# Optimization experiments

Hardware: AMD Instinct MI355X
Metric: run time of the kernel (lower is better)

## Reference

```python
import jax, jax.numpy as jnp
import numpy as np

G = 8          # deformable groups
K = 9          # 3x3 kernel points
MAXR = 10.0    # max_residue_magnitude


def conv2d(x, w, b):
    # x: [B,Cin,H,W], w: [Cout,Cin,3,3], SAME padding, stride 1
    y = jax.lax.conv_general_dilated(x, w, (1, 1), ((1, 1), (1, 1)),
                                     dimension_numbers=('NCHW', 'OIHW', 'NCHW'))
    return y + b[None, :, None, None]


def lrelu(x):
    return jnp.where(x >= 0, x, 0.1 * x)


def offset_branch(x, ws, bs):
    for w, b in zip(ws[:-1], bs[:-1]):
        x = lrelu(conv2d(x, w, b))
    return conv2d(x, ws[-1], bs[-1])


def mdcn(x, offset, mask, w, b):
    # Modulated deformable conv, 3x3, stride 1, pad 1, dilation 1, groups=1.
    # offset: [B, G*K*2, H, W] ordered (g, k, (y,x)); mask: [B, G*K, H, W]
    B, C, H, W = x.shape
    Cg = C // G
    off = offset.reshape(B, G, K, 2, H, W)
    m = mask.reshape(B, G, K, H, W)
    ky = (jnp.arange(K) // 3 - 1).astype(x.dtype)   # kernel dy, pad=1
    kx = (jnp.arange(K) % 3 - 1).astype(x.dtype)    # kernel dx
    hy = jnp.arange(H, dtype=x.dtype)
    wx = jnp.arange(W, dtype=x.dtype)
    py = hy[None, None, None, :, None] + ky[None, None, :, None, None] + off[:, :, :, 0]  # [B,G,K,H,W]
    px = wx[None, None, None, None, :] + kx[None, None, :, None, None] + off[:, :, :, 1]
    y0f = jnp.floor(py); x0f = jnp.floor(px)
    ly = py - y0f; lx = px - x0f
    y0 = y0f.astype(jnp.int32); x0 = x0f.astype(jnp.int32)
    xf = x.reshape(B, G, Cg, H * W)

    def gather(yi, xi):
        valid = ((yi >= 0) & (yi < H) & (xi >= 0) & (xi < W)).astype(x.dtype)
        yc = jnp.clip(yi, 0, H - 1)
        xc = jnp.clip(xi, 0, W - 1)
        idx = (yc * W + xc).reshape(B, G, 1, K * H * W)
        v = jnp.take_along_axis(xf, idx, axis=3).reshape(B, G, Cg, K, H, W)
        return v * valid.reshape(B, G, 1, K, H, W)

    ly_ = ly[:, :, None]; lx_ = lx[:, :, None]  # [B,G,1,K,H,W]
    samp = (gather(y0, x0) * (1 - ly_) * (1 - lx_)
            + gather(y0, x0 + 1) * (1 - ly_) * lx_
            + gather(y0 + 1, x0) * ly_ * (1 - lx_)
            + gather(y0 + 1, x0 + 1) * ly_ * lx_)
    samp = samp * m[:, :, None]                 # modulation
    wr = w.reshape(w.shape[0], G, Cg, K)        # [Cout,G,Cg,K]
    return jnp.einsum('ogck,bgckhw->bohw', wr, samp) + b[None, :, None, None]


def setup_inputs():
    key = jax.random.key(0)
    ks = jax.random.split(key, 40)
    B, C, H, W = 1, 64, 256, 256
    s = 0.05
    inp = {
        'feat_prev': jax.random.normal(ks[0], (B, C, H, W), jnp.float32),
        'feat_next': jax.random.normal(ks[1], (B, C, H, W), jnp.float32),
        'extra_feat_prev': jax.random.normal(ks[2], (B, 2 * C, H, W), jnp.float32),
        'extra_feat_next': jax.random.normal(ks[3], (B, 2 * C, H, W), jnp.float32),
        'flow_prev': jax.random.normal(ks[4], (B, 2, H, W), jnp.float32),
        'flow_next': jax.random.normal(ks[5], (B, 2, H, W), jnp.float32),
    }
    shapes = [(C, 2 * C, 3, 3), (C, C, 3, 3), (C, C, 3, 3), (27 * G, C, 3, 3)]
    i = 6
    for pre in ('off1', 'off2'):
        for j, sh in enumerate(shapes):
            inp[f'{pre}_w{j}'] = jax.random.normal(ks[i], sh, jnp.float32) * s; i += 1
            inp[f'{pre}_b{j}'] = jax.random.normal(ks[i], (sh[0],), jnp.float32) * s; i += 1
    inp['dcn1_w'] = jax.random.normal(ks[i], (C, C, 3, 3), jnp.float32) * s; i += 1
    inp['dcn1_b'] = jax.random.normal(ks[i], (C,), jnp.float32) * s; i += 1
    inp['dcn2_w'] = jax.random.normal(ks[i], (C, C, 3, 3), jnp.float32) * s; i += 1
    inp['dcn2_b'] = jax.random.normal(ks[i], (C,), jnp.float32) * s; i += 1
    inp['fus_w'] = jax.random.normal(ks[i], (C, 2 * C, 3, 3), jnp.float32) * s; i += 1
    inp['fus_b'] = jax.random.normal(ks[i], (C,), jnp.float32) * s
    return inp


def reference(feat_prev, feat_next, extra_feat_prev, extra_feat_next, flow_prev, flow_next,
              off1_w0, off1_b0, off1_w1, off1_b1, off1_w2, off1_b2, off1_w3, off1_b3,
              off2_w0, off2_b0, off2_w1, off2_b1, off2_w2, off2_b2, off2_w3, off2_b3,
              dcn1_w, dcn1_b, dcn2_w, dcn2_b, fus_w, fus_b):
    def branch(feat, extra, flow, ws, bs, dw, db):
        out = offset_branch(extra, ws, bs)
        o1, o2, msk = jnp.split(out, 3, axis=1)
        off = MAXR * jnp.tanh(jnp.concatenate([o1, o2], axis=1))
        off = off + jnp.tile(flow[:, ::-1], (1, off.shape[1] // 2, 1, 1))  # flip(1).repeat
        msk = jax.nn.sigmoid(msk)
        return mdcn(feat, off, msk, dw, db)

    fp = branch(feat_prev, extra_feat_prev, flow_prev,
                [off1_w0, off1_w1, off1_w2, off1_w3], [off1_b0, off1_b1, off1_b2, off1_b3],
                dcn1_w, dcn1_b)
    fn = branch(feat_next, extra_feat_next, flow_next,
                [off2_w0, off2_w1, off2_w2, off2_w3], [off2_b0, off2_b1, off2_b2, off2_b3],
                dcn2_w, dcn2_b)
    return conv2d(jnp.concatenate([fp, fn], axis=1), fus_w, fus_b)
```

## Files before the change

### kernel.cpp

```cpp
#include <hip/hip_runtime.h>
#include <cstddef>
#include <cstdint>

constexpr int IMG = 256;
constexpr int NPIX = 65536;
constexpr int PW = 258;
constexpr size_t PREC = (size_t)PW * PW;

typedef _Float16 h8 __attribute__((ext_vector_type(8)));
typedef float f32x4 __attribute__((ext_vector_type(4)));

template<int CIN>
__device__ __forceinline__ void zero_pad_rec(int i, _Float16* buf)
{
  constexpr int Q = CIN / 8;
  if (i >= 1028 * Q) return;
  int pr = i / Q, qi = i - pr * Q;
  int rec;
  if (pr < 258) rec = pr;
  else if (pr < 516) rec = 257 * 258 + (pr - 258);
  else { int j = pr - 516; rec = (1 + (j >> 1)) * 258 + ((j & 1) ? 257 : 0); }
  *reinterpret_cast<uint4*>(&buf[(size_t)rec * CIN + qi * 8]) = uint4{0, 0, 0, 0};
}

template<int CIN>
__global__ __launch_bounds__(256) void zeropad_k(_Float16* __restrict__ buf)
{
  zero_pad_rec<CIN>(blockIdx.x * 256 + threadIdx.x, buf);
}

template<int CIN>
__global__ __launch_bounds__(256) void prep_hwc_k(
    const float* __restrict__ in0, const float* __restrict__ in1,
    _Float16* __restrict__ out0, _Float16* __restrict__ out1)
{
  const int z = blockIdx.z;
  const float* in = z ? in1 : in0;
  _Float16* out = z ? out1 : out0;
  int b = blockIdx.x;
  if (b >= 256) { zero_pad_rec<CIN>((b - 256) * 256 + threadIdx.x, out); return; }
  int pix = b * 256 + threadIdx.x;
  int py = pix >> 8, px = pix & 255;
  size_t rec = ((size_t)(py + 1) * PW + px + 1) * CIN;
#pragma unroll
  for (int c0 = 0; c0 < CIN; c0 += 8) {
    _Float16 t[8];
#pragma unroll
    for (int j = 0; j < 8; ++j)
      t[j] = (_Float16)in[(size_t)(c0 + j) * NPIX + pix];
    *reinterpret_cast<uint4*>(&out[rec + c0]) = *reinterpret_cast<uint4*>(t);
  }
}

__device__ __forceinline__ void wfrag(
    const float* __restrict__ w, int cin_tot, int cin_off, int KC, int NBF,
    int nvalid, int idx, _Float16* __restrict__ oHi, _Float16* __restrict__ oLo)
{
  int l = idx & 63;
  int r = idx >> 6;
  int fg = r % NBF; r /= NBF;
  int c = r % KC;
  int t = r / KC;
  int n = fg * 16 + (l & 15);
  int cinb = c * 32 + (l >> 4) * 8;
  _Float16 vh[8], vl[8];
#pragma unroll
  for (int j = 0; j < 8; ++j) {
    float x = 0.f;
    if (n < nvalid) x = w[((size_t)n * cin_tot + cin_off + cinb + j) * 9 + t];
    vh[j] = (_Float16)x;
    vl[j] = (_Float16)(x - (float)vh[j]);
  }
  *reinterpret_cast<uint4*>(oHi + (size_t)idx * 8) = *reinterpret_cast<uint4*>(vh);
  if (oLo)
    *reinterpret_cast<uint4*>(oLo + (size_t)idx * 8) = *reinterpret_cast<uint4*>(vl);
}

__global__ __launch_bounds__(256) void wprep_all_k(
    const float* __restrict__ w0, const float* __restrict__ w1,
    const float* __restrict__ w2, const float* __restrict__ w3,
    const float* __restrict__ wf, const float* __restrict__ dw,
    _Float16* b0h, _Float16* b0l, _Float16* b1h, _Float16* b1l,
    _Float16* b2h, _Float16* b2l, _Float16* b3h, _Float16* b3l,
    _Float16* bfh, _Float16* __restrict__ wB)
{
  int idx = blockIdx.x * 256 + threadIdx.x;
  if (idx < 9216)       wfrag(w0, 128, 0, 4, 4, 64, idx, b0h, b0l);
  else if (idx < 13824) wfrag(w1, 64, 0, 2, 4, 64, idx - 9216, b1h, b1l);
  else if (idx < 18432) wfrag(w2, 64, 0, 2, 4, 64, idx - 13824, b2h, b2l);
  else if (idx < 36864) wfrag(w3, 64, 0, 2, 16, 216, idx - 18432, b3h, b3l);
  else if (idx < 41472) {
    int i = idx - 36864;
    int l = i & 63;
    int r = i >> 6;
    int f = r & 3;
    int p = r >> 2;
    int t = p * 4 + (l >> 4);
    int g = (t * 57) >> 9;
    int k = t - 9 * g;
    int n = f * 16 + (l & 15);
    _Float16 v[8];
#pragma unroll
    for (int j = 0; j < 8; ++j)
      v[j] = (_Float16)dw[(size_t)n * 576 + g * 72 + j * 9 + k];
    *reinterpret_cast<uint4*>(wB + (size_t)i * 8) = *reinterpret_cast<uint4*>(v);
  }
  else if (wf && idx < 50688)
    wfrag(wf, 128, 0, 4, 4, 64, idx - 41472, bfh, nullptr);
}

template<int CIN, int EPI, bool DBL, typename OT>
__global__ __launch_bounds__(256) void conv_mfma_k(
    const _Float16* __restrict__ act0, const _Float16* __restrict__ act1,
    const _Float16* __restrict__ wHi0, const _Float16* __restrict__ wHi1,
    const _Float16* __restrict__ wLo0, const _Float16* __restrict__ wLo1,
    const float* __restrict__ bias0, const float* __restrict__ bias1,
    OT* __restrict__ out0, OT* __restrict__ out1, int ncout, int NBF)
{
  constexpr int Q = CIN / 8;
  constexpr int KC = CIN / 32;
  constexpr int NT = DBL ? 2 : 1;
  constexpr int NREC = 198;
  __shared__ __align__(16) _Float16 sA[NREC * CIN];

  const int z = blockIdx.z;
  const _Float16* __restrict__ act = z ? act1 : act0;
  const _Float16* __restrict__ wHi = z ? wHi1 : wHi0;
  const _Float16* __restrict__ wLo = z ? wLo1 : wLo0;
  const float* __restrict__ bias = z ? bias1 : bias0;
  OT* __restrict__ out = z ? out1 : out0;

  const int tid = threadIdx.x;
  const int lane = tid & 63;
  const int wv = tid >> 6;
  const int b = blockIdx.x;
  const int inner = b >> 3;
  const int y = (b & 7) * 32 + (inner & 31);
  const int x0 = (inner >> 5) << 6;
  const int n0 = blockIdx.y << 6;

  for (int i = tid; i < NREC * Q; i += 256) {
    int rec = i / Q, q = i - rec * Q;
    int seg = rec / 66, xr = rec - seg * 66;
    size_t g = ((size_t)(y + seg) * PW + x0 + xr) * CIN + q * 8;
    int slot = (q + rec) & (Q - 1);
    *reinterpret_cast<uint4*>(&sA[rec * CIN + slot * 8]) =
        *reinterpret_cast<const uint4*>(&act[g]);
  }

  const int fgb = (n0 >> 4) + wv;
  auto bload = [&](int t, int c, const _Float16* src) {
    return *reinterpret_cast<const h8*>(
        &src[((((size_t)t * KC + c) * NBF + fgb) * 64 + lane) * 8]);
  };
  h8 Bn[KC][NT];
#pragma unroll
  for (int c = 0; c < KC; ++c) {
    Bn[c][0] = bload(0, c, wHi);
    if (DBL) Bn[c][1] = bload(0, c, wLo);
  }

  f32x4 acc[4];
#pragma unroll
  for (int a = 0; a < 4; ++a) acc[a] = f32x4{0.f, 0.f, 0.f, 0.f};
  __syncthreads();

  const int m = lane & 15, kq = lane >> 4;
#pragma unroll 1
  for (int t = 0; t < 9; ++t) {
    h8 Bc[KC][NT];
#pragma unroll
    for (int c = 0; c < KC; ++c) {
      Bc[c][0] = Bn[c][0];
      if (DBL) Bc[c][1] = Bn[c][1];
    }
    if (t < 8) {
#pragma unroll
      for (int c = 0; c < KC; ++c) {
        Bn[c][0] = bload(t + 1, c, wHi);
        if (DBL) Bn[c][1] = bload(t + 1, c, wLo);
      }
    }
    const int lrb = (t / 3) * 66 + (t % 3) + m;
#pragma unroll
    for (int c = 0; c < KC; ++c) {
      const int q = c * 4 + kq;
#pragma unroll
      for (int mf = 0; mf < 4; ++mf) {
        int lr = lrb + mf * 16;
        int slot = (q + lr) & (Q - 1);
        h8 ah = *reinterpret_cast<const h8*>(&sA[lr * CIN + slot * 8]);
        acc[mf] = __builtin_amdgcn_mfma_f32_16x16x32_f16(
            ah, Bc[c][0], acc[mf], 0, 0, 0);
        if (DBL)
          acc[mf] = __builtin_amdgcn_mfma_f32_16x16x32_f16(
              ah, Bc[c][1], acc[mf], 0, 0, 0);
      }
    }
  }

  if (EPI == 0) {
    const int ch = wv * 16 + m;
    const float bv = bias[ch];
#pragma unroll
    for (int mf = 0; mf < 4; ++mf)
#pragma unroll
      for (int r = 0; r < 4; ++r) {
        int p = mf * 16 + kq * 4 + r;
        float v = acc[mf][r] + bv;
        v = (v >= 0.f) ? v : 0.1f * v;
        reinterpret_cast<_Float16*>(out)[((size_t)(y + 1) * PW + x0 + p + 1) * 64 + ch] =
            (_Float16)v;
      }
  } else {
    __syncthreads();
    float* sF = reinterpret_cast<float*>(sA);
    const int nl = wv * 16 + m;
#pragma unroll
    for (int mf = 0; mf < 4; ++mf) {
      int ml = mf * 16 + kq * 4;
      f32x4 v = acc[mf];
      float bv = (n0 + nl < ncout) ? bias[n0 + nl] : 0.f;
      v[0] += bv; v[1] += bv; v[2] += bv; v[3] += bv;
      *reinterpret_cast<f32x4*>(&sF[nl * 68 + ml]) = v;
    }
    __syncthreads();
    for (int i = tid; i < 1024; i += 256) {
      int row = i >> 4, cx = (i & 15) * 4;
      int gc = n0 + row;
      if (gc < ncout) {
        f32x4 v = *reinterpret_cast<f32x4*>(&sF[row * 68 + cx]);
        size_t ob = (size_t)gc * NPIX + (size_t)y * IMG + x0 + cx;
        if (sizeof(OT) == 2) {
          _Float16 t4[4] = {(_Float16)v[0], (_Float16)v[1],
                            (_Float16)v[2], (_Float16)v[3]};
          *reinterpret_cast<uint2*>(reinterpret_cast<_Float16*>(out) + ob) =
              *reinterpret_cast<uint2*>(t4);
        } else {
          *reinterpret_cast<f32x4*>(reinterpret_cast<float*>(out) + ob) = v;
        }
      }
    }
  }
}

__global__ __launch_bounds__(256) void featg_k(
    const float* __restrict__ in0, const float* __restrict__ in1,
    _Float16* __restrict__ out0, _Float16* __restrict__ out1)
{
  const int z = blockIdx.z;
  const float* in = z ? in1 : in0;
  _Float16* out = z ? out1 : out0;
  int pix = blockIdx.x * 256 + threadIdx.x;
#pragma unroll
  for (int g = 0; g < 8; ++g) {
    _Float16 t[8];
#pragma unroll
    for (int c = 0; c < 8; ++c)
      t[c] = (_Float16)in[(size_t)(g * 8 + c) * NPIX + pix];
    *reinterpret_cast<uint4*>(&out[((size_t)g * NPIX + pix) * 8]) =
        *reinterpret_cast<uint4*>(t);
  }
}

struct GS {
  h8 a, b, c, d;
  _Float16 w00, w01, w10, w11;
  float r0, r1, r2;
  h8 bf0, bf1, bf2, bf3;
};

__global__ __launch_bounds__(256, 8) void mdcn_mfma_k(
    const _Float16* __restrict__ featG0, const _Float16* __restrict__ featG1,
    const _Float16* __restrict__ o2160, const _Float16* __restrict__ o2161,
    const float* __restrict__ flow0, const float* __restrict__ flow1,
    const _Float16* __restrict__ wB0, const _Float16* __restrict__ wB1,
    const float* __restrict__ bias0, const float* __restrict__ bias1,
    _Float16* __restrict__ actF)
{
  const int z = blockIdx.z;
  const char* __restrict__ featGc =
      reinterpret_cast<const char*>(z ? featG1 : featG0);
  const char* __restrict__ o216c =
      reinterpret_cast<const char*>(z ? o2161 : o2160);
  const float* __restrict__ flow = z ? flow1 : flow0;
  const char* __restrict__ wBc = reinterpret_cast<const char*>(z ? wB1 : wB0);
  const float* __restrict__ bias = z ? bias1 : bias0;
  const int zoff = z << 6;

  const int tid = threadIdx.x;
  const int lane = tid & 63;
  const int wv = tid >> 6;
  const int b = blockIdx.x;
  const int inner = b >> 3;
  const int row = (b & 7) * 32 + (inner & 31);
  const int xseg = inner >> 5;
  const int m = lane & 15;
  const int tq = lane >> 4;
  const int xw = xseg * 64 + wv * 16;
  const int x = xw + m;
  const int pix = row * 256 + x;

  const float fy = flow[NPIX + pix];
  const float fx = flow[pix];
  const float rowf = (float)row, xf = (float)x;

  f32x4 acc[4];
#pragma unroll
  for (int f = 0; f < 4; ++f) acc[f] = f32x4{0.f, 0.f, 0.f, 0.f};

  uint32_t ro0 = ((uint32_t)(2 * tq) * NPIX + (uint32_t)pix) * 2;
  uint32_t ro2 = ((uint32_t)(144 + tq) * NPIX + (uint32_t)pix) * 2;
  auto rawloadv = [&](float& a0, float& a1, float& a2) {
    a0 = (float)*reinterpret_cast<const _Float16*>(o216c + ro0);
    a1 = (float)*reinterpret_cast<const _Float16*>(o216c + ro0 + NPIX * 2);
    a2 = (float)*reinterpret_cast<const _Float16*>(o216c + ro2);
    ro0 += 8u * NPIX * 2;
    ro2 += 4u * NPIX * 2;
  };

  auto setup = [&](int p, float s0, float s1, float s2, GS& o) {
    const int t = p * 4 + tq;
    const int g = (t * 57) >> 9;
    const int k = t - 9 * g;
    const int kd = (k * 11) >> 5;
    const int km = k - 3 * kd;
    const float mm = __builtin_amdgcn_rcpf(1.f + __expf(-s2));
    const float e0 = __expf(2.f * s0);
    const float e1 = __expf(2.f * s1);
    const float th0 = 1.f - 2.f * __builtin_amdgcn_rcpf(e0 + 1.f);
    const float th1 = 1.f - 2.f * __builtin_amdgcn_rcpf(e1 + 1.f);
    const float pyf = rowf + (float)(kd - 1) + 10.f * th0 + fy;
    const float pxf = xf + (float)(km - 1) + 10.f * th1 + fx;
    const float y0f = floorf(pyf), x0f = floorf(pxf);
    const float ly = pyf - y0f, lx = pxf - x0f;
    const int y0 = (int)y0f, x0i = (int)x0f;
    const int y1 = y0 + 1, x1 = x0i + 1;
    const bool vy0 = (unsigned)y0 < (unsigned)IMG, vy1 = (unsigned)y1 < (unsigned)IMG;
    const bool vx0 = (unsigned)x0i < (unsigned)IMG, vx1 = (unsigned)x1 < (unsigned)IMG;
    const int y0c = min(max(y0, 0), IMG - 1), y1c = min(max(y1, 0), IMG - 1);
    const int x0c = min(max(x0i, 0), IMG - 1), x1c = min(max(x1, 0), IMG - 1);
    const float oy = 1.f - ly, ox = 1.f - lx;
    const float py0 = oy * mm, py1 = ly * mm;
    const float w00 = (vy0 && vx0) ? py0 * ox : 0.f;
    const float w01 = (vy0 && vx1) ? py0 * lx : 0.f;
    const float w10 = (vy1 && vx0) ? py1 * ox : 0.f;
    const float w11 = (vy1 && vx1) ? py1 * lx : 0.f;
    o.w00 = (_Float16)w00; o.w01 = (_Float16)w01;
    o.w10 = (_Float16)w10; o.w11 = (_Float16)w11;
    const uint32_t gb = ((uint32_t)g << 16);
    const uint32_t ry0 = gb + ((uint32_t)y0c << 8);
    const uint32_t ry1 = gb + ((uint32_t)y1c << 8);
    o.a = *reinterpret_cast<const h8*>(featGc + ((ry0 + x0c) << 4));
    o.b = *reinterpret_cast<const h8*>(featGc + ((ry0 + x1c) << 4));
    o.c = *reinterpret_cast<const h8*>(featGc + ((ry1 + x0c) << 4));
    o.d = *reinterpret_cast<const h8*>(featGc + ((ry1 + x1c) << 4));
  };

  const uint32_t lane16 = (uint32_t)lane * 16;
  auto bfload = [&](int p, GS& o) {
    const uint32_t w = (uint32_t)p * 4096 + lane16;
    o.bf0 = *reinterpret_cast<const h8*>(wBc + w);
    o.bf1 = *reinterpret_cast<const h8*>(wBc + w + 1024);
    o.bf2 = *reinterpret_cast<const h8*>(wBc + w + 2048);
    o.bf3 = *reinterpret_cast<const h8*>(wBc + w + 3072);
  };

  auto consume = [&](GS& cur) {
    h8 af = cur.a * cur.w00 + cur.b * cur.w01 +
            cur.c * cur.w10 + cur.d * cur.w11;
    acc[0] = __builtin_amdgcn_mfma_f32_16x16x32_f16(af, cur.bf0, acc[0], 0, 0, 0);
    acc[1] = __builtin_amdgcn_mfma_f32_16x16x32_f16(af, cur.bf1, acc[1], 0, 0, 0);
    acc[2] = __builtin_amdgcn_mfma_f32_16x16x32_f16(af, cur.bf2, acc[2], 0, 0, 0);
    acc[3] = __builtin_amdgcn_mfma_f32_16x16x32_f16(af, cur.bf3, acc[3], 0, 0, 0);
  };

  auto body = [&](int p, GS& cur, GS& nxt) {
    setup(p + 1, nxt.r0, nxt.r1, nxt.r2, nxt);
    rawloadv(cur.r0, cur.r1, cur.r2);
    bfload(p + 1, nxt);
    consume(cur);
  };

  GS A, B;
  {
    float t0, t1, t2;
    rawloadv(t0, t1, t2);
    rawloadv(B.r0, B.r1, B.r2);
    bfload(0, A);
    setup(0, t0, t1, t2, A);
  }

#pragma unroll 1
  for (int it = 0; it < 8; ++it) {
    body(2 * it, A, B);
    body(2 * it + 1, B, A);
  }
  setup(17, B.r0, B.r1, B.r2, B);
  bfload(17, B);
  consume(A);
  consume(B);

  const size_t rb = ((size_t)(row + 1) * PW + xw + 1) * 128 + zoff;
#pragma unroll
  for (int f = 0; f < 4; ++f) {
    const int ch = f * 16 + m;
    const float bv = bias[ch];
#pragma unroll
    for (int r = 0; r < 4; ++r)
      actF[rb + (size_t)(tq * 4 + r) * 128 + ch] = (_Float16)(acc[f][r] + bv);
  }
}

extern "C" void kernel_launch(void* const* d_in, const int* in_sizes, int n_in,
                              void* d_out, int out_size, void* d_ws, size_t ws_size,
                              hipStream_t stream)
{
  const float* feat[2]  = {(const float*)d_in[0], (const float*)d_in[1]};
  const float* extra[2] = {(const float*)d_in[2], (const float*)d_in[3]};
  const float* flow[2]  = {(const float*)d_in[4], (const float*)d_in[5]};
  const float* ow[2][4];
  const float* ob[2][4];
  for (int br = 0; br < 2; ++br)
    for (int j = 0; j < 4; ++j) {
      ow[br][j] = (const float*)d_in[6 + br * 8 + j * 2];
      ob[br][j] = (const float*)d_in[6 + br * 8 + j * 2 + 1];
    }
  const float* dcnw[2] = {(const float*)d_in[22], (const float*)d_in[24]};
  const float* dcnb[2] = {(const float*)d_in[23], (const float*)d_in[25]};
  const float* fusw = (const float*)d_in[26];
  const float* fusb = (const float*)d_in[27];

  char* wsb = (char*)d_ws;
  size_t off = 0;
  auto alloc = [&](size_t bytes) {
    void* p = wsb + off;
    off += (bytes + 255) & ~(size_t)255;
    return p;
  };
  _Float16* R1 = (_Float16*)alloc(PREC * 128 * 2 * 2);
  _Float16* actI0 = R1;
  _Float16* actI1 = R1 + PREC * 128;
  _Float16* actB0 = R1;
  _Float16* actB1 = R1 + PREC * 64;
  _Float16* actF  = R1;
  _Float16* R2 = (_Float16*)alloc(PREC * 64 * 2 * 2);
  _Float16* actA0 = R2;
  _Float16* actA1 = R2 + PREC * 64;
  _Float16* featG0 = R2;
  _Float16* featG1 = R2 + PREC * 64;
  _Float16* o2160 = (_Float16*)alloc((size_t)216 * NPIX * 2 * 2);
  _Float16* o2161 = o2160 + (size_t)216 * NPIX;
  _Float16* wB0 = (_Float16*)alloc(73728 * 2);
  _Float16* wB1 = wB0 + 36864;
  _Float16* wb0h[2] = {(_Float16*)alloc(147456), (_Float16*)alloc(147456)};
  _Float16* wb0l[2] = {(_Float16*)alloc(147456), (_Float16*)alloc(147456)};
  _Float16* wb1h[2] = {(_Float16*)alloc(73728), (_Float16*)alloc(73728)};
  _Float16* wb1l[2] = {(_Float16*)alloc(73728), (_Float16*)alloc(73728)};
  _Float16* wb2h[2] = {(_Float16*)alloc(73728), (_Float16*)alloc(73728)};
  _Float16* wb2l[2] = {(_Float16*)alloc(73728), (_Float16*)alloc(73728)};
  _Float16* wb3h[2] = {(_Float16*)alloc(294912), (_Float16*)alloc(294912)};
  _Float16* wb3l[2] = {(_Float16*)alloc(294912), (_Float16*)alloc(294912)};
  _Float16* wbFh = (_Float16*)alloc(147456);
  float* outp = (float*)d_out;

  dim3 blk256(256);
  zeropad_k<64><<<dim3(33), blk256, 0, stream>>>(actA0);
  zeropad_k<64><<<dim3(33), blk256, 0, stream>>>(actA1);

  wprep_all_k<<<dim3(198), blk256, 0, stream>>>(
      ow[0][0], ow[0][1], ow[0][2], ow[0][3], fusw, dcnw[0],
      wb0h[0], wb0l[0], wb1h[0], wb1l[0], wb2h[0], wb2l[0],
      wb3h[0], wb3l[0], wbFh, wB0);
  wprep_all_k<<<dim3(162), blk256, 0, stream>>>(
      ow[1][0], ow[1][1], ow[1][2], ow[1][3], nullptr, dcnw[1],
      wb0h[1], wb0l[1], wb1h[1], wb1l[1], wb2h[1], wb2l[1],
      wb3h[1], wb3l[1], nullptr, wB1);

  prep_hwc_k<128><<<dim3(321, 1, 2), blk256, 0, stream>>>(
      extra[0], extra[1], actI0, actI1);

  conv_mfma_k<128, 0, true, _Float16><<<dim3(1024, 1, 2), blk256, 0, stream>>>(
      actI0, actI1, wb0h[0], wb0h[1], wb0l[0], wb0l[1],
      ob[0][0], ob[1][0], actA0, actA1, 64, 4);
  zeropad_k<64><<<dim3(33), blk256, 0, stream>>>(actB0);
  zeropad_k<64><<<dim3(33), blk256, 0, stream>>>(actB1);
  conv_mfma_k<64, 0, true, _Float16><<<dim3(1024, 1, 2), blk256, 0, stream>>>(
      actA0, actA1, wb1h[0], wb1h[1], wb1l[0], wb1l[1],
      ob[0][1], ob[1][1], actB0, actB1, 64, 4);
  conv_mfma_k<64, 0, true, _Float16><<<dim3(1024, 1, 2), blk256, 0, stream>>>(
      actB0, actB1, wb2h[0], wb2h[1], wb2l[0], wb2l[1],
      ob[0][2], ob[1][2], actA0, actA1, 64, 4);
  zeropad_k<128><<<dim3(65), blk256, 0, stream>>>(actF);
  conv_mfma_k<64, 1, true, _Float16><<<dim3(1024, 4, 2), blk256, 0, stream>>>(
      actA0, actA1, wb3h[0], wb3h[1], wb3l[0], wb3l[1],
      ob[0][3], ob[1][3], o2160, o2161, 216, 16);

  featg_k<<<dim3(256, 1, 2), blk256, 0, stream>>>(
      feat[0], feat[1], featG0, featG1);
  mdcn_mfma_k<<<dim3(1024, 1, 2), blk256, 0, stream>>>(
      featG0, featG1, o2160, o2161, flow[0], flow[1],
      wB0, wB1, dcnb[0], dcnb[1], actF);

  conv_mfma_k<128, 1, false, float><<<dim3(1024, 1, 1), blk256, 0, stream>>>(
      actF, actF, wbFh, wbFh, nullptr, nullptr,
      fusb, fusb, outp, outp, 64, 4);
}
```

Baseline: 531.0 us.

## Stage MDCN weight fragments through triple-buffered LDS shared across waves

Each wave used to load the full 4 KB weight B-fragment for every kernel step from global memory into registers. Now the four waves each load a quarter of it, store it into a three-slot shared-memory ring, and every wave reads the whole fragment back from LDS before its MFMAs. This removes the redundant per-wave global weight traffic and the register copies of the fragments held in the pipelined state struct. In exchange it adds a block-wide barrier at every step, which can stall waves that would otherwise overlap their gather latency. The launch-bounds occupancy hint is also lowered from 8 to 4.

```diff
diff --git a/kernel.cpp b/kernel.cpp
--- a/kernel.cpp
+++ b/kernel.cpp
@@ -267,10 +267,9 @@
   h8 a, b, c, d;
   _Float16 w00, w01, w10, w11;
   float r0, r1, r2;
-  h8 bf0, bf1, bf2, bf3;
 };
 
-__global__ __launch_bounds__(256, 8) void mdcn_mfma_k(
+__global__ __launch_bounds__(256, 4) void mdcn_mfma_k(
     const _Float16* __restrict__ featG0, const _Float16* __restrict__ featG1,
     const _Float16* __restrict__ o2160, const _Float16* __restrict__ o2161,
     const float* __restrict__ flow0, const float* __restrict__ flow1,
@@ -278,6 +277,8 @@
     const float* __restrict__ bias0, const float* __restrict__ bias1,
     _Float16* __restrict__ actF)
 {
+  __shared__ __align__(16) _Float16 sWB[3 * 2048];
+
   const int z = blockIdx.z;
   const char* __restrict__ featGc =
       reinterpret_cast<const char*>(z ? featG1 : featG0);
@@ -304,6 +305,9 @@
   const float fy = flow[NPIX + pix];
   const float fx = flow[pix];
   const float rowf = (float)row, xf = (float)x;
+  const uint32_t wvb = (uint32_t)wv << 10;
+  const uint32_t lane16 = (uint32_t)lane * 16;
+  const int wvh = wv << 9;
 
   f32x4 acc[4];
 #pragma unroll
@@ -357,49 +361,58 @@
     o.d = *reinterpret_cast<const h8*>(featGc + ((ry1 + x1c) << 4));
   };
 
-  const uint32_t lane16 = (uint32_t)lane * 16;
-  auto bfload = [&](int p, GS& o) {
-    const uint32_t w = (uint32_t)p * 4096 + lane16;
-    o.bf0 = *reinterpret_cast<const h8*>(wBc + w);
-    o.bf1 = *reinterpret_cast<const h8*>(wBc + w + 1024);
-    o.bf2 = *reinterpret_cast<const h8*>(wBc + w + 2048);
-    o.bf3 = *reinterpret_cast<const h8*>(wBc + w + 3072);
-  };
-
-  auto consume = [&](GS& cur) {
+  auto consume = [&](GS& cur, int bufi) {
+    const _Float16* wp = &sWB[bufi * 2048 + lane * 8];
+    h8 bf0 = *reinterpret_cast<const h8*>(wp);
+    h8 bf1 = *reinterpret_cast<const h8*>(wp + 512);
+    h8 bf2 = *reinterpret_cast<const h8*>(wp + 1024);
+    h8 bf3 = *reinterpret_cast<const h8*>(wp + 1536);
     h8 af = cur.a * cur.w00 + cur.b * cur.w01 +
             cur.c * cur.w10 + cur.d * cur.w11;
-    acc[0] = __builtin_amdgcn_mfma_f32_16x16x32_f16(af, cur.bf0, acc[0], 0, 0, 0);
-    acc[1] = __builtin_amdgcn_mfma_f32_16x16x32_f16(af, cur.bf1, acc[1], 0, 0, 0);
-    acc[2] = __builtin_amdgcn_mfma_f32_16x16x32_f16(af, cur.bf2, acc[2], 0, 0, 0);
-    acc[3] = __builtin_amdgcn_mfma_f32_16x16x32_f16(af, cur.bf3, acc[3], 0, 0, 0);
+    acc[0] = __builtin_amdgcn_mfma_f32_16x16x32_f16(af, bf0, acc[0], 0, 0, 0);
+    acc[1] = __builtin_amdgcn_mfma_f32_16x16x32_f16(af, bf1, acc[1], 0, 0, 0);
+    acc[2] = __builtin_amdgcn_mfma_f32_16x16x32_f16(af, bf2, acc[2], 0, 0, 0);
+    acc[3] = __builtin_amdgcn_mfma_f32_16x16x32_f16(af, bf3, acc[3], 0, 0, 0);
   };
 
-  auto body = [&](int p, GS& cur, GS& nxt) {
+  auto body = [&](int p, int bc, GS& cur, GS& nxt) {
+    const int bs = (bc == 2) ? 0 : bc + 1;
+    h8 tw = *reinterpret_cast<const h8*>(
+        wBc + (size_t)(p + 1) * 4096 + wvb + lane16);
+    rawloadv(cur.r0, cur.r1, cur.r2);
+    *reinterpret_cast<h8*>(&sWB[bs * 2048 + wvh + lane * 8]) = tw;
+    __syncthreads();
     setup(p + 1, nxt.r0, nxt.r1, nxt.r2, nxt);
-    rawloadv(cur.r0, cur.r1, cur.r2);
-    bfload(p + 1, nxt);
-    consume(cur);
+    consume(cur, bc);
   };
 
   GS A, B;
   {
+    h8 tw = *reinterpret_cast<const h8*>(wBc + wvb + lane16);
     float t0, t1, t2;
     rawloadv(t0, t1, t2);
     rawloadv(B.r0, B.r1, B.r2);
-    bfload(0, A);
+    *reinterpret_cast<h8*>(&sWB[wvh + lane * 8]) = tw;
     setup(0, t0, t1, t2, A);
   }
 
+  int bc = 0;
 #pragma unroll 1
   for (int it = 0; it < 8; ++it) {
-    body(2 * it, A, B);
-    body(2 * it + 1, B, A);
-  }
-  setup(17, B.r0, B.r1, B.r2, B);
-  bfload(17, B);
-  consume(A);
-  consume(B);
+    body(2 * it, bc, A, B);
+    bc = (bc == 2) ? 0 : bc + 1;
+    body(2 * it + 1, bc, B, A);
+    bc = (bc == 2) ? 0 : bc + 1;
+  }
+  {
+    h8 tw = *reinterpret_cast<const h8*>(
+        wBc + (size_t)17 * 4096 + wvb + lane16);
+    setup(17, B.r0, B.r1, B.r2, B);
+    *reinterpret_cast<h8*>(&sWB[2 * 2048 + wvh + lane * 8]) = tw;
+    __syncthreads();
+    consume(A, 1);
+    consume(B, 2);
+  }
 
   const size_t rb = ((size_t)(row + 1) * PW + xw + 1) * 128 + zoff;
 #pragma unroll
```

New measurement: 488.4 us. -8.0%, faster.
